# Kernel tuning notes

Hardware: AMD Instinct MI355X
Metric: run time of the kernel (lower is better)

The kernel has to match this reference:

```python
import jax, jax.numpy as jnp
import numpy as np

# ---- module config (from init_kwargs) ----
DIM = 2048
NUM_HEADS = 16
NUM_KV_HEADS = 4
HEAD_DIM = DIM // NUM_HEADS          # 128
KV_DIM = NUM_KV_HEADS * HEAD_DIM     # 512
ROPE_BASE = 10000.0
EPS = 1e-5  # TrainableBitNetLinear.eps (assumed standard BitNet clamp)


def _quant_matmul(x2, w, eps=EPS):
    """Dynamic int8 quantized matmul: per-row absmax weight quant + per-token absmax act quant.
    x2: [N, in], w: [out, in]. Returns (out [N, out], dequantized weight [out, in])."""
    w_scale = jnp.maximum(jnp.max(jnp.abs(w), axis=1) / 127.0, eps)            # [out]
    wq = jnp.clip(jnp.round(w / w_scale[:, None]), -127.0, 127.0)              # int8 codes (kept float)
    a_scale = jnp.maximum(jnp.max(jnp.abs(x2), axis=1) / 127.0, eps)           # [N] dynamic per-row
    xq = jnp.clip(jnp.round(x2 / a_scale[:, None]), -127.0, 127.0)
    out = (xq @ wq.T) * (a_scale[:, None] * w_scale[None, :])
    return out, wq * w_scale[:, None]


@jax.custom_vjp
def int8_ste_linear(x, w):
    x2 = x.reshape(-1, x.shape[-1])
    out, _ = _quant_matmul(x2, w)
    return out.reshape(*x.shape[:-1], w.shape[0])


def _ste_fwd(x, w):
    x2 = x.reshape(-1, x.shape[-1])
    out, w_dq = _quant_matmul(x2, w)
    return out.reshape(*x.shape[:-1], w.shape[0]), (x, w_dq)


def _ste_bwd(res, g):
    # STE: grad_x = g @ W_dequant ; grad_w = g.T @ x (raw float x, matching torch backward)
    x, w_dq = res
    g2 = g.reshape(-1, g.shape[-1])
    x2 = x.reshape(-1, x.shape[-1])
    return (g2 @ w_dq).reshape(x.shape), g2.T @ x2


int8_ste_linear.defvjp(_ste_fwd, _ste_bwd)


def _rms_norm(x):
    # F.rms_norm with no weight: eps defaults to dtype eps
    eps = jnp.finfo(x.dtype).eps
    return x * jax.lax.rsqrt(jnp.mean(jnp.square(x), axis=-1, keepdims=True) + eps)


def _rope_tables(seqlen, dtype):
    inv_freq = 1.0 / (ROPE_BASE ** (jnp.arange(0, HEAD_DIM, 2, dtype=jnp.float32) / HEAD_DIM))  # [half]
    t = jnp.arange(seqlen, dtype=jnp.float32)
    freqs = jnp.outer(t, inv_freq)                        # [S, half]
    return jnp.cos(freqs).astype(dtype), jnp.sin(freqs).astype(dtype)


def _apply_rotary(x, cos, sin):
    # x: [B, H, S, hd]; cos/sin: [S, hd/2] broadcast over B,H
    half = x.shape[-1] // 2
    x1, x2 = x[..., :half], x[..., half:]
    return jnp.concatenate((x1 * cos + x2 * sin, x1 * -sin + x2 * cos), axis=-1)


def setup_inputs() -> dict:
    key = jax.random.key(0)
    kx, kq, kk, kv, ko = jax.random.split(key, 5)
    x = jax.random.normal(kx, (2, 2048, DIM), dtype=jnp.float32)
    w_q = jax.random.normal(kq, (DIM, DIM), dtype=jnp.float32) * 0.125
    w_k = jax.random.normal(kk, (KV_DIM, DIM), dtype=jnp.float32) * 0.125
    w_v = jax.random.normal(kv, (KV_DIM, DIM), dtype=jnp.float32) * 0.125
    w_o = jax.random.normal(ko, (DIM, DIM), dtype=jnp.float32) * 0.125
    q_gain = jnp.full((NUM_HEADS,), 1.0, dtype=jnp.float32)
    return {"x": x, "w_q": w_q, "w_k": w_k, "w_v": w_v, "w_o": w_o, "q_gain": q_gain}


def reference(x, w_q, w_k, w_v, w_o, q_gain):
    B, S, D = x.shape
    G = NUM_HEADS // NUM_KV_HEADS
    # fused QKV: per-row quant of concatenated weights == per-weight quant then concat
    fused = int8_ste_linear(x, jnp.concatenate((w_q, w_k, w_v), axis=0))  # [B, S, D+2*KV_DIM]
    q_raw, k_raw, v_raw = jnp.split(fused, [D, D + KV_DIM], axis=-1)
    q = q_raw.reshape(B, S, NUM_HEADS, HEAD_DIM).transpose(0, 2, 1, 3)     # [B, H, S, hd]
    k = k_raw.reshape(B, S, NUM_KV_HEADS, HEAD_DIM).transpose(0, 2, 1, 3)  # [B, Hk, S, hd]
    v = v_raw.reshape(B, S, NUM_KV_HEADS, HEAD_DIM).transpose(0, 2, 1, 3)
    q = _rms_norm(q)
    k = _rms_norm(k)
    cos, sin = _rope_tables(S, q.dtype)
    q = _apply_rotary(q, cos, sin)
    k = _apply_rotary(k, cos, sin)
    q = q * q_gain[None, :, None, None]
    # GQA causal attention (SDPA enable_gqa semantics), scale = 1/sqrt(head_dim)
    qg = q.reshape(B, NUM_KV_HEADS, G, S, HEAD_DIM)
    scale = 1.0 / jnp.sqrt(jnp.asarray(HEAD_DIM, dtype=q.dtype))
    scores = jnp.einsum('bkgqd,bkld->bkgql', qg, k) * scale                # [B, Hk, G, S, S]
    causal = jnp.tril(jnp.ones((S, S), dtype=bool))
    scores = jnp.where(causal, scores, jnp.finfo(scores.dtype).min)
    attn = jax.nn.softmax(scores, axis=-1)
    y = jnp.einsum('bkgql,bkld->bkgqd', attn, v)                           # [B, Hk, G, S, hd]
    y = y.reshape(B, NUM_HEADS, S, HEAD_DIM).transpose(0, 2, 1, 3).reshape(B, S, D)
    return int8_ste_linear(y, w_o)
```

## Files before the change

kernel.cpp:

```cpp
#include <hip/hip_runtime.h>
#include <hip/hip_fp16.h>

typedef unsigned short u16;
typedef __attribute__((ext_vector_type(8))) _Float16 f16x8;
typedef __attribute__((ext_vector_type(4))) float f32x4;

static __device__ __forceinline__ u16 f2h(float f) {
    __half h = __float2half(f);
    return __half_as_ushort(h);
}

__global__ __launch_bounds__(256) void k_rope_tables(float* __restrict__ ct, float* __restrict__ st) {
    int idx = blockIdx.x * 256 + threadIdx.x;
    int s = idx >> 6, i = idx & 63;
    float inv = 1.0f / powf(10000.0f, (float)i * (1.0f / 64.0f));
    float f = (float)s * inv;
    ct[idx] = cosf(f);
    st[idx] = sinf(f);
}

__global__ __launch_bounds__(256) void k_quant_rows(const float* __restrict__ src,
        u16* __restrict__ dst, float* __restrict__ scales) {
    int row = blockIdx.x;
    const float* p = src + (size_t)row * 2048;
    int t = threadIdx.x;
    float4 v0 = ((const float4*)p)[t * 2 + 0];
    float4 v1 = ((const float4*)p)[t * 2 + 1];
    float amax = fmaxf(
        fmaxf(fmaxf(fabsf(v0.x), fabsf(v0.y)), fmaxf(fabsf(v0.z), fabsf(v0.w))),
        fmaxf(fmaxf(fabsf(v1.x), fabsf(v1.y)), fmaxf(fabsf(v1.z), fabsf(v1.w))));
#pragma unroll
    for (int d = 1; d < 64; d <<= 1) amax = fmaxf(amax, __shfl_xor(amax, d, 64));
    __shared__ float red[4];
    if ((t & 63) == 0) red[t >> 6] = amax;
    __syncthreads();
    amax = fmaxf(fmaxf(red[0], red[1]), fmaxf(red[2], red[3]));
    float scl = fmaxf(amax * (1.0f / 127.0f), 1e-5f);
    if (t == 0) scales[row] = scl;
    float vv[8] = {v0.x, v0.y, v0.z, v0.w, v1.x, v1.y, v1.z, v1.w};
    u16 q[8];
#pragma unroll
    for (int j = 0; j < 8; ++j) {
        float r = rintf(vv[j] / scl);
        r = fminf(fmaxf(r, -127.0f), 127.0f);
        q[j] = f2h(r);
    }
    *(uint4*)&dst[(size_t)row * 2048 + t * 8] = *(uint4*)q;
}

#define BM 128
#define BN 128
#define BK 64
#define LDSP 72

__global__ __launch_bounds__(256) void k_gemm_q(const u16* __restrict__ A,
        const u16* __restrict__ B, const float* __restrict__ ascale,
        const float* __restrict__ wscale, float* __restrict__ out,
        int M, int N, int K) {
    __shared__ u16 As[BM][LDSP];
    __shared__ u16 Bs[BN][LDSP];
    int t = threadIdx.x;
    int wid = t >> 6, lane = t & 63;
    int bm = blockIdx.y * BM, bn = blockIdx.x * BN;
    int wm = (wid >> 1) * 64, wn = (wid & 1) * 64;
    int rl = lane & 15, kg = lane >> 4;

    f32x4 z = {0.f, 0.f, 0.f, 0.f};
    f32x4 acc[4][4];
#pragma unroll
    for (int i = 0; i < 4; ++i)
#pragma unroll
        for (int j = 0; j < 4; ++j) acc[i][j] = z;

    int sr = t >> 3, sc = (t & 7) * 8;
    const u16* Ab = A + (size_t)(bm + sr) * K + sc;
    const u16* Bb = B + (size_t)(bn + sr) * K + sc;
    uint4 ra[4], rb[4];
#pragma unroll
    for (int p = 0; p < 4; ++p) {
        ra[p] = *(const uint4*)(Ab + (size_t)p * 32 * K);
        rb[p] = *(const uint4*)(Bb + (size_t)p * 32 * K);
    }
    int NT = K / BK;
    for (int kt = 0; kt < NT; ++kt) {
#pragma unroll
        for (int p = 0; p < 4; ++p) {
            *(uint4*)&As[sr + p * 32][sc] = ra[p];
            *(uint4*)&Bs[sr + p * 32][sc] = rb[p];
        }
        __syncthreads();
        if (kt + 1 < NT) {
            size_t koff = (size_t)(kt + 1) * BK;
#pragma unroll
            for (int p = 0; p < 4; ++p) {
                ra[p] = *(const uint4*)(Ab + (size_t)p * 32 * K + koff);
                rb[p] = *(const uint4*)(Bb + (size_t)p * 32 * K + koff);
            }
        }
#pragma unroll
        for (int ks = 0; ks < 2; ++ks) {
            f16x8 af[4], bfr[4];
#pragma unroll
            for (int i = 0; i < 4; ++i)
                af[i] = *(const f16x8*)&As[wm + i * 16 + rl][ks * 32 + kg * 8];
#pragma unroll
            for (int j = 0; j < 4; ++j)
                bfr[j] = *(const f16x8*)&Bs[wn + j * 16 + rl][ks * 32 + kg * 8];
#pragma unroll
            for (int i = 0; i < 4; ++i)
#pragma unroll
                for (int j = 0; j < 4; ++j)
                    acc[i][j] = __builtin_amdgcn_mfma_f32_16x16x32_f16(af[i], bfr[j], acc[i][j], 0, 0, 0);
        }
        __syncthreads();
    }
#pragma unroll
    for (int i = 0; i < 4; ++i) {
#pragma unroll
        for (int j = 0; j < 4; ++j) {
            int n = bn + wn + j * 16 + rl;
            float wsn = wscale[n];
#pragma unroll
            for (int r = 0; r < 4; ++r) {
                int m = bm + wm + i * 16 + kg * 4 + r;
                out[(size_t)m * N + n] = acc[i][j][r] * ascale[m] * wsn;
            }
        }
    }
}

__global__ __launch_bounds__(256) void k_rmsrope(const float* __restrict__ qkv,
        const float* __restrict__ qgain, const float* __restrict__ ct,
        const float* __restrict__ st, u16* __restrict__ qb,
        u16* __restrict__ kb, u16* __restrict__ vb) {
    int wave = blockIdx.x * 4 + (threadIdx.x >> 6);
    int lane = threadIdx.x & 63;
    int token = wave / 24, unit = wave - token * 24;
    int b = token >> 11, s = token & 2047;
    int col;
    if (unit < 16) col = unit * 128;
    else if (unit < 20) col = 2048 + (unit - 16) * 128;
    else col = 2560 + (unit - 20) * 128;
    const float* p = qkv + (size_t)token * 3072 + col;
    float x1 = p[lane], x2 = p[lane + 64];
    if (unit < 20) {
        float ss = x1 * x1 + x2 * x2;
#pragma unroll
        for (int d = 1; d < 64; d <<= 1) ss += __shfl_xor(ss, d, 64);
        float rn = rsqrtf(ss * (1.0f / 128.0f) + 1.1920929e-07f);
        x1 *= rn; x2 *= rn;
        float c = ct[s * 64 + lane], sn = st[s * 64 + lane];
        float o1 = x1 * c + x2 * sn;
        float o2 = x2 * c - x1 * sn;
        if (unit < 16) {
            float g = qgain[unit] * 0.08838834764831845f;
            o1 *= g; o2 *= g;
        }
        x1 = o1; x2 = o2;
    }
    u16 u1 = f2h(x1), u2 = f2h(x2);
    size_t off; u16* dst;
    if (unit < 16)      { dst = qb; off = ((size_t)(b * 16 + unit) * 2048 + s) * 128; }
    else if (unit < 20) { dst = kb; off = ((size_t)(b * 4 + (unit - 16)) * 2048 + s) * 128; }
    else                { dst = vb; off = ((size_t)(b * 4 + (unit - 20)) * 2048 + s) * 128; }
    dst[off + lane] = u1;
    dst[off + lane + 64] = u2;
}

__global__ __launch_bounds__(256) void k_transpose_v(const u16* __restrict__ vb,
        u16* __restrict__ vt) {
    __shared__ u16 tls[64][72];
    int bh = blockIdx.x;
    int s0 = blockIdx.y * 64;
    int d0 = blockIdx.z * 64;
    const u16* src = vb + (size_t)bh * 2048 * 128;
    u16* dst = vt + (size_t)bh * 128 * 2048;
    int r = threadIdx.x >> 3, c = (threadIdx.x & 7) * 8;
#pragma unroll
    for (int p = 0; p < 2; ++p) {
        uint4 d4 = *(const uint4*)&src[(size_t)(s0 + r + p * 32) * 128 + d0 + c];
        u16 tmp[8]; *(uint4*)tmp = d4;
#pragma unroll
        for (int j = 0; j < 8; ++j) tls[c + j][r + p * 32] = tmp[j];
    }
    __syncthreads();
#pragma unroll
    for (int p = 0; p < 2; ++p) {
        int dd = r + p * 32;
        u16 tmp[8];
#pragma unroll
        for (int j = 0; j < 8; ++j) tmp[j] = tls[dd][c + j];
        *(uint4*)&dst[(size_t)(d0 + dd) * 2048 + s0 + c] = *(uint4*)tmp;
    }
}

__global__ __launch_bounds__(256) void k_attn(const u16* __restrict__ qb,
        const u16* __restrict__ kb, const u16* __restrict__ vt,
        float* __restrict__ y) {
    int pair = blockIdx.x, h = blockIdx.y, b = blockIdx.z;
    int wid = threadIdx.x >> 6, lane = threadIdx.x & 63;
    int kvh = h >> 2;
    int rl = lane & 15, kg = lane >> 4;
    const u16* kp = kb + (size_t)(b * 4 + kvh) * 2048 * 128;
    const u16* vp = vt + (size_t)(b * 4 + kvh) * 128 * 2048;
    __shared__ u16 Ps[4][16][40];
    f32x4 z = {0.f, 0.f, 0.f, 0.f};

    for (int phase = 0; phase < 2; ++phase) {
        int qc = (phase == 0) ? pair : (31 - pair);
        int q0 = qc * 64 + wid * 16;
        const u16* qp = qb + ((size_t)(b * 16 + h) * 2048 + q0) * 128;

        f16x8 qf[4];
#pragma unroll
        for (int kc = 0; kc < 4; ++kc)
            qf[kc] = *(const f16x8*)&qp[(size_t)rl * 128 + kc * 32 + kg * 8];

        f32x4 o[8];
#pragma unroll
        for (int j = 0; j < 8; ++j) o[j] = z;
        float mrow[4], lrow[4];
#pragma unroll
        for (int r = 0; r < 4; ++r) { mrow[r] = -3.0e38f; lrow[r] = 0.f; }

        int nsteps = (q0 + 47) >> 5;

        auto STEP = [&](int tstep, f16x8 (&kcur)[2][4], f16x8 (&knxt)[2][4]) {
            int kv0 = tstep * 32;
            f16x8 vf[8];
#pragma unroll
            for (int j = 0; j < 8; ++j)
                vf[j] = *(const f16x8*)&vp[(size_t)(j * 16 + rl) * 2048 + kv0 + kg * 8];
            f32x4 sc[2];
#pragma unroll
            for (int nt = 0; nt < 2; ++nt) {
                f32x4 acc = z;
#pragma unroll
                for (int kc = 0; kc < 4; ++kc)
                    acc = __builtin_amdgcn_mfma_f32_16x16x32_f16(qf[kc], kcur[nt][kc], acc, 0, 0, 0);
                sc[nt] = acc;
            }
            if (tstep + 1 < nsteps) {
                int kn0 = kv0 + 32;
#pragma unroll
                for (int nt = 0; nt < 2; ++nt)
#pragma unroll
                    for (int kc = 0; kc < 4; ++kc)
                        knxt[nt][kc] = *(const f16x8*)&kp[(size_t)(kn0 + nt * 16 + rl) * 128 + kc * 32 + kg * 8];
            }
            float alpha[4];
#pragma unroll
            for (int r = 0; r < 4; ++r) {
                int grow = q0 + kg * 4 + r;
                float s0v = sc[0][r], s1v = sc[1][r];
                if (kv0 + rl > grow) s0v = -3.0e38f;
                if (kv0 + 16 + rl > grow) s1v = -3.0e38f;
                float mx = fmaxf(s0v, s1v);
                mx = fmaxf(mx, __shfl_xor(mx, 1, 64));
                mx = fmaxf(mx, __shfl_xor(mx, 2, 64));
                mx = fmaxf(mx, __shfl_xor(mx, 4, 64));
                mx = fmaxf(mx, __shfl_xor(mx, 8, 64));
                float mnew = fmaxf(mrow[r], mx);
                float a = __expf(mrow[r] - mnew);
                s0v = __expf(s0v - mnew);
                s1v = __expf(s1v - mnew);
                sc[0][r] = s0v; sc[1][r] = s1v;
                float rs = s0v + s1v;
                rs += __shfl_xor(rs, 1, 64);
                rs += __shfl_xor(rs, 2, 64);
                rs += __shfl_xor(rs, 4, 64);
                rs += __shfl_xor(rs, 8, 64);
                lrow[r] = lrow[r] * a + rs;
                mrow[r] = mnew;
                alpha[r] = a;
            }
#pragma unroll
            for (int j = 0; j < 8; ++j) {
                o[j][0] *= alpha[0];
                o[j][1] *= alpha[1];
                o[j][2] *= alpha[2];
                o[j][3] *= alpha[3];
            }
#pragma unroll
            for (int nt = 0; nt < 2; ++nt)
#pragma unroll
                for (int r = 0; r < 4; ++r)
                    Ps[wid][kg * 4 + r][nt * 16 + rl] = f2h(sc[nt][r]);
            f16x8 pa = *(const f16x8*)&Ps[wid][rl][kg * 8];
#pragma unroll
            for (int j = 0; j < 8; ++j)
                o[j] = __builtin_amdgcn_mfma_f32_16x16x32_f16(pa, vf[j], o[j], 0, 0, 0);
        };

        f16x8 kfA[2][4], kfB[2][4];
#pragma unroll
        for (int nt = 0; nt < 2; ++nt)
#pragma unroll
            for (int kc = 0; kc < 4; ++kc)
                kfA[nt][kc] = *(const f16x8*)&kp[(size_t)(nt * 16 + rl) * 128 + kc * 32 + kg * 8];

        for (int tstep = 0; tstep < nsteps; tstep += 2) {
            STEP(tstep, kfA, kfB);
            if (tstep + 1 < nsteps) STEP(tstep + 1, kfB, kfA);
        }

#pragma unroll
        for (int r = 0; r < 4; ++r) lrow[r] = 1.0f / lrow[r];
#pragma unroll
        for (int j = 0; j < 8; ++j)
#pragma unroll
            for (int r = 0; r < 4; ++r) {
                int grow = q0 + kg * 4 + r;
                y[(size_t)(b * 2048 + grow) * 2048 + h * 128 + j * 16 + rl] = o[j][r] * lrow[r];
            }
    }
}

extern "C" void kernel_launch(void* const* d_in, const int* in_sizes, int n_in,
                              void* d_out, int out_size, void* d_ws, size_t ws_size,
                              hipStream_t stream) {
    const float* x     = (const float*)d_in[0];
    const float* w_q   = (const float*)d_in[1];
    const float* w_k   = (const float*)d_in[2];
    const float* w_v   = (const float*)d_in[3];
    const float* w_o   = (const float*)d_in[4];
    const float* qgain = (const float*)d_in[5];
    float* out = (float*)d_out;

    char* ws = (char*)d_ws;
    size_t off = 0;
    auto alloc = [&](size_t bytes) {
        char* p = ws + off;
        off += (bytes + 255) & ~(size_t)255;
        return (void*)p;
    };
    u16*   wqf  = (u16*)  alloc(3072ull * 2048 * 2);
    u16*   wqo  = (u16*)  alloc(2048ull * 2048 * 2);
    float* wsc  = (float*)alloc(5120 * 4);
    float* asc  = (float*)alloc(4096 * 4);
    float* ysc  = (float*)alloc(4096 * 4);
    float* ctab = (float*)alloc(2048ull * 64 * 4);
    float* stab = (float*)alloc(2048ull * 64 * 4);
    u16*   xq   = (u16*)  alloc(4096ull * 2048 * 2);
    float* qkv  = (float*)alloc(4096ull * 3072 * 4);
    u16*   qbuf = (u16*)  alloc(2ull * 16 * 2048 * 128 * 2);
    u16*   kbuf = (u16*)  alloc(2ull * 4 * 2048 * 128 * 2);
    u16*   vbuf = (u16*)  alloc(2ull * 4 * 2048 * 128 * 2);
    u16*   vtb  = (u16*)  alloc(2ull * 4 * 128 * 2048 * 2);
    (void)ws_size; (void)in_sizes; (void)n_in; (void)out_size;

    k_rope_tables<<<512, 256, 0, stream>>>(ctab, stab);
    k_quant_rows<<<2048, 256, 0, stream>>>(w_q, wqf, wsc);
    k_quant_rows<<<512, 256, 0, stream>>>(w_k, wqf + 2048ull * 2048, wsc + 2048);
    k_quant_rows<<<512, 256, 0, stream>>>(w_v, wqf + 2560ull * 2048, wsc + 2560);
    k_quant_rows<<<2048, 256, 0, stream>>>(w_o, wqo, wsc + 3072);
    k_quant_rows<<<4096, 256, 0, stream>>>(x, xq, asc);

    k_gemm_q<<<dim3(3072 / BN, 4096 / BM), 256, 0, stream>>>(xq, wqf, asc, wsc, qkv, 4096, 3072, 2048);
    k_rmsrope<<<(4096 * 24) / 4, 256, 0, stream>>>(qkv, qgain, ctab, stab, qbuf, kbuf, vbuf);
    k_transpose_v<<<dim3(8, 32, 2), 256, 0, stream>>>(vbuf, vtb);

    float* ybuf = qkv;
    k_attn<<<dim3(16, 16, 2), 256, 0, stream>>>(qbuf, kbuf, vtb, ybuf);

    u16* yq = xq;
    k_quant_rows<<<4096, 256, 0, stream>>>(ybuf, yq, ysc);
    k_gemm_q<<<dim3(2048 / BN, 4096 / BM), 256, 0, stream>>>(yq, wqo, ysc, wsc + 3072, out, 4096, 2048, 2048);
}
```

Baseline: 661.9 us.

## Split attention KV range across warps with shared-memory merge of partial softmax

The attention kernel now gives each block a single 16-row query tile per phase, and its four warps split the KV steps among themselves (split-K within the block) instead of each warp owning its own query rows. The partial max, sum and output of each warp are merged through shared memory before a vectorised store. The QK and PV MFMAs are transposed so each lane holds one query row, which removes most cross-lane shuffles in the softmax. The grid grows fourfold and launch bounds request three blocks per CU. The change adds shared-memory traffic, two barriers per phase, and drops the double-buffered K prefetch.

Result: no change. 665.6 us (+0.6%).

```diff
diff --git a/kernel.cpp b/kernel.cpp
--- a/kernel.cpp
+++ b/kernel.cpp
@@ -2,6 +2,7 @@
 #include <hip/hip_fp16.h>
 
 typedef unsigned short u16;
+typedef unsigned int u32;
 typedef __attribute__((ext_vector_type(8))) _Float16 f16x8;
 typedef __attribute__((ext_vector_type(4))) float f32x4;
 
@@ -194,21 +195,24 @@
     }
 }
 
-__global__ __launch_bounds__(256) void k_attn(const u16* __restrict__ qb,
+__global__ __launch_bounds__(256, 3) void k_attn(const u16* __restrict__ qb,
         const u16* __restrict__ kb, const u16* __restrict__ vt,
         float* __restrict__ y) {
-    int pair = blockIdx.x, h = blockIdx.y, b = blockIdx.z;
+    int pr = blockIdx.x, h = blockIdx.y, b = blockIdx.z;
     int wid = threadIdx.x >> 6, lane = threadIdx.x & 63;
     int kvh = h >> 2;
     int rl = lane & 15, kg = lane >> 4;
     const u16* kp = kb + (size_t)(b * 4 + kvh) * 2048 * 128;
     const u16* vp = vt + (size_t)(b * 4 + kvh) * 128 * 2048;
-    __shared__ u16 Ps[4][16][40];
+
+    __shared__ __align__(16) u16 Ps[4][16][56];
+    __shared__ float om[4][16][132];
+    __shared__ float mlm[4][2][16];
     f32x4 z = {0.f, 0.f, 0.f, 0.f};
 
     for (int phase = 0; phase < 2; ++phase) {
-        int qc = (phase == 0) ? pair : (31 - pair);
-        int q0 = qc * 64 + wid * 16;
+        int qc = phase ? (127 - pr) : pr;
+        int q0 = qc * 16;
         const u16* qp = qb + ((size_t)(b * 16 + h) * 2048 + q0) * 128;
 
         f16x8 qf[4];
@@ -219,14 +223,18 @@
         f32x4 o[8];
 #pragma unroll
         for (int j = 0; j < 8; ++j) o[j] = z;
-        float mrow[4], lrow[4];
-#pragma unroll
-        for (int r = 0; r < 4; ++r) { mrow[r] = -3.0e38f; lrow[r] = 0.f; }
-
+        float m = -3.0e38f, l = 0.f;
+        int qrow = q0 + rl;
         int nsteps = (q0 + 47) >> 5;
 
-        auto STEP = [&](int tstep, f16x8 (&kcur)[2][4], f16x8 (&knxt)[2][4]) {
-            int kv0 = tstep * 32;
+        for (int t = wid; t < nsteps; t += 4) {
+            int kv0 = t * 32;
+            f16x8 kf[2][4];
+#pragma unroll
+            for (int nt = 0; nt < 2; ++nt)
+#pragma unroll
+                for (int kc = 0; kc < 4; ++kc)
+                    kf[nt][kc] = *(const f16x8*)&kp[(size_t)(kv0 + nt * 16 + rl) * 128 + kc * 32 + kg * 8];
             f16x8 vf[8];
 #pragma unroll
             for (int j = 0; j < 8; ++j)
@@ -237,82 +245,73 @@
                 f32x4 acc = z;
 #pragma unroll
                 for (int kc = 0; kc < 4; ++kc)
-                    acc = __builtin_amdgcn_mfma_f32_16x16x32_f16(qf[kc], kcur[nt][kc], acc, 0, 0, 0);
+                    acc = __builtin_amdgcn_mfma_f32_16x16x32_f16(kf[nt][kc], qf[kc], acc, 0, 0, 0);
                 sc[nt] = acc;
             }
-            if (tstep + 1 < nsteps) {
-                int kn0 = kv0 + 32;
-#pragma unroll
-                for (int nt = 0; nt < 2; ++nt)
-#pragma unroll
-                    for (int kc = 0; kc < 4; ++kc)
-                        knxt[nt][kc] = *(const f16x8*)&kp[(size_t)(kn0 + nt * 16 + rl) * 128 + kc * 32 + kg * 8];
-            }
-            float alpha[4];
-#pragma unroll
-            for (int r = 0; r < 4; ++r) {
-                int grow = q0 + kg * 4 + r;
-                float s0v = sc[0][r], s1v = sc[1][r];
-                if (kv0 + rl > grow) s0v = -3.0e38f;
-                if (kv0 + 16 + rl > grow) s1v = -3.0e38f;
-                float mx = fmaxf(s0v, s1v);
-                mx = fmaxf(mx, __shfl_xor(mx, 1, 64));
-                mx = fmaxf(mx, __shfl_xor(mx, 2, 64));
-                mx = fmaxf(mx, __shfl_xor(mx, 4, 64));
-                mx = fmaxf(mx, __shfl_xor(mx, 8, 64));
-                float mnew = fmaxf(mrow[r], mx);
-                float a = __expf(mrow[r] - mnew);
-                s0v = __expf(s0v - mnew);
-                s1v = __expf(s1v - mnew);
-                sc[0][r] = s0v; sc[1][r] = s1v;
-                float rs = s0v + s1v;
-                rs += __shfl_xor(rs, 1, 64);
-                rs += __shfl_xor(rs, 2, 64);
-                rs += __shfl_xor(rs, 4, 64);
-                rs += __shfl_xor(rs, 8, 64);
-                lrow[r] = lrow[r] * a + rs;
-                mrow[r] = mnew;
-                alpha[r] = a;
-            }
-#pragma unroll
-            for (int j = 0; j < 8; ++j) {
-                o[j][0] *= alpha[0];
-                o[j][1] *= alpha[1];
-                o[j][2] *= alpha[2];
-                o[j][3] *= alpha[3];
-            }
+            int thr = qrow - kv0 - kg * 4;
 #pragma unroll
             for (int nt = 0; nt < 2; ++nt)
 #pragma unroll
                 for (int r = 0; r < 4; ++r)
-                    Ps[wid][kg * 4 + r][nt * 16 + rl] = f2h(sc[nt][r]);
-            f16x8 pa = *(const f16x8*)&Ps[wid][rl][kg * 8];
+                    if (nt * 16 + r > thr) sc[nt][r] = -3.0e38f;
+            float pm = fmaxf(
+                fmaxf(fmaxf(sc[0][0], sc[0][1]), fmaxf(sc[0][2], sc[0][3])),
+                fmaxf(fmaxf(sc[1][0], sc[1][1]), fmaxf(sc[1][2], sc[1][3])));
+            pm = fmaxf(pm, __shfl_xor(pm, 16, 64));
+            pm = fmaxf(pm, __shfl_xor(pm, 32, 64));
+            float mnew = fmaxf(m, pm);
+            float alpha = __expf(m - mnew);
+            float p[8];
+#pragma unroll
+            for (int nt = 0; nt < 2; ++nt)
+#pragma unroll
+                for (int r = 0; r < 4; ++r)
+                    p[nt * 4 + r] = __expf(sc[nt][r] - mnew);
+            float rs = ((p[0] + p[1]) + (p[2] + p[3])) + ((p[4] + p[5]) + (p[6] + p[7]));
+            rs += __shfl_xor(rs, 16, 64);
+            rs += __shfl_xor(rs, 32, 64);
+            l = l * alpha + rs;
+            m = mnew;
+#pragma unroll
+            for (int j = 0; j < 8; ++j) o[j] *= alpha;
+#pragma unroll
+            for (int nt = 0; nt < 2; ++nt) {
+                u32 pk0 = (u32)f2h(p[nt * 4 + 0]) | ((u32)f2h(p[nt * 4 + 1]) << 16);
+                u32 pk1 = (u32)f2h(p[nt * 4 + 2]) | ((u32)f2h(p[nt * 4 + 3]) << 16);
+                *(u32*)&Ps[wid][rl][nt * 16 + kg * 4]     = pk0;
+                *(u32*)&Ps[wid][rl][nt * 16 + kg * 4 + 2] = pk1;
+            }
+            f16x8 pB = *(const f16x8*)&Ps[wid][rl][kg * 8];
 #pragma unroll
             for (int j = 0; j < 8; ++j)
-                o[j] = __builtin_amdgcn_mfma_f32_16x16x32_f16(pa, vf[j], o[j], 0, 0, 0);
-        };
-
-        f16x8 kfA[2][4], kfB[2][4];
-#pragma unroll
-        for (int nt = 0; nt < 2; ++nt)
-#pragma unroll
-            for (int kc = 0; kc < 4; ++kc)
-                kfA[nt][kc] = *(const f16x8*)&kp[(size_t)(nt * 16 + rl) * 128 + kc * 32 + kg * 8];
-
-        for (int tstep = 0; tstep < nsteps; tstep += 2) {
-            STEP(tstep, kfA, kfB);
-            if (tstep + 1 < nsteps) STEP(tstep + 1, kfB, kfA);
-        }
-
-#pragma unroll
-        for (int r = 0; r < 4; ++r) lrow[r] = 1.0f / lrow[r];
+                o[j] = __builtin_amdgcn_mfma_f32_16x16x32_f16(vf[j], pB, o[j], 0, 0, 0);
+        }
+        if (kg == 0) { mlm[wid][0][rl] = m; mlm[wid][1][rl] = l; }
 #pragma unroll
         for (int j = 0; j < 8; ++j)
-#pragma unroll
-            for (int r = 0; r < 4; ++r) {
-                int grow = q0 + kg * 4 + r;
-                y[(size_t)(b * 2048 + grow) * 2048 + h * 128 + j * 16 + rl] = o[j][r] * lrow[r];
-            }
+            *(f32x4*)&om[wid][rl][j * 16 + kg * 4] = o[j];
+        __syncthreads();
+        float mw[4], lw[4];
+#pragma unroll
+        for (int w = 0; w < 4; ++w) { mw[w] = mlm[w][0][rl]; lw[w] = mlm[w][1][rl]; }
+        float M = fmaxf(fmaxf(mw[0], mw[1]), fmaxf(mw[2], mw[3]));
+        float aw[4], lsum = 0.f;
+#pragma unroll
+        for (int w = 0; w < 4; ++w) { aw[w] = __expf(mw[w] - M); lsum += aw[w] * lw[w]; }
+        float linv = 1.0f / lsum;
+        int d0 = wid * 32 + kg * 8;
+#pragma unroll
+        for (int seg = 0; seg < 2; ++seg) {
+            f32x4 acc = z;
+#pragma unroll
+            for (int w = 0; w < 4; ++w) {
+                f32x4 v = *(const f32x4*)&om[w][rl][d0 + seg * 4];
+                acc += aw[w] * v;
+            }
+            acc *= linv;
+            *(f32x4*)&y[(size_t)(b * 2048 + q0 + rl) * 2048 + h * 128 + d0 + seg * 4] = acc;
+        }
+        __syncthreads();
     }
 }
 
@@ -361,7 +360,7 @@
     k_transpose_v<<<dim3(8, 32, 2), 256, 0, stream>>>(vbuf, vtb);
 
     float* ybuf = qkv;
-    k_attn<<<dim3(16, 16, 2), 256, 0, stream>>>(qbuf, kbuf, vtb, ybuf);
+    k_attn<<<dim3(64, 16, 2), 256, 0, stream>>>(qbuf, kbuf, vtb, ybuf);
 
     u16* yq = xq;
     k_quant_rows<<<4096, 256, 0, stream>>>(ybuf, yq, ysc);
```
